# Performance work log

Hardware: AMD Instinct MI355X
Metric: run time of the kernel (lower is better)

Reference implementation:

```python
import jax, jax.numpy as jnp
import numpy as np

B, T, D = 128, 512, 400
N_VALS, N_ACTS = 1024, 128

def setup_inputs() -> dict:
    key = jax.random.key(0)
    ks = jax.random.split(key, 7)
    H_utt = jax.random.normal(ks[0], (B, T, D), dtype=jnp.float32)
    c_utt = jax.random.normal(ks[1], (B, D), dtype=jnp.float32)
    C_acts = jax.random.normal(ks[2], (B, N_ACTS, D), dtype=jnp.float32)
    C_vals = jax.random.normal(ks[3], (N_VALS, 1, D), dtype=jnp.float32)
    W_score = jax.random.normal(ks[4], (1, D), dtype=jnp.float32) * (1.0 / np.sqrt(D))
    b_score = jnp.zeros((1,), dtype=jnp.float32)
    lens = jax.random.randint(ks[5], (B,), T // 2, T + 1, dtype=jnp.int64 if jax.config.read('jax_enable_x64') else jnp.int32)
    lens = lens.at[0].set(T)  # ensure max(lens) == T so masking matches torch semantics
    return {"H_utt": H_utt, "c_utt": c_utt, "C_acts": C_acts, "C_vals": C_vals,
            "W_score": W_score, "b_score": b_score, "utterance_len": lens}

def reference(H_utt, c_utt, C_acts, C_vals, W_score, b_score, utterance_len):
    vals = C_vals[:, 0, :]                                   # [V, D]
    # --- y_utts: default attention of each value vector over utterance states ---
    scores = jnp.einsum('btd,vd->bvt', H_utt, vals)          # mul+sum scoring
    mask = jnp.arange(T)[None, :] < utterance_len[:, None]   # [B, T]
    scores = jnp.where(mask[:, None, :], scores, -jnp.inf)
    probs = jax.nn.softmax(scores, axis=-1)                  # [B, V, T]
    q_utts = jnp.einsum('bvt,btd->bvd', probs, H_utt)        # weighted sum contexts
    y_utts = jnp.einsum('bvd,d->bv', q_utts, W_score[0]) + b_score[0]  # utt_scorer
    # --- y_acts: attention of c_utt over per-example act vectors, then score vs vals ---
    s2 = jnp.einsum('bad,bd->ba', C_acts, c_utt)
    p2 = jax.nn.softmax(s2, axis=-1)
    q_acts = jnp.einsum('ba,bad->bd', p2, C_acts)            # [B, D]
    y_acts = q_acts @ vals.T                                 # [B, V]
    return (y_utts, y_acts)
```

## Files before the change

kernel.cpp:

```cpp
#include <hip/hip_runtime.h>
#include <hip/hip_bf16.h>

#define B_  128
#define T_  512
#define D_  400
#define NV  1024
#define NA  128

#define LDH  424
#define NT   32
#define MV   128
#define LOG2E 1.4426950408889634f

typedef __bf16 bf16_t;
typedef bf16_t bf16x8 __attribute__((ext_vector_type(8)));
typedef bf16_t bf16x4 __attribute__((ext_vector_type(4)));
typedef float  floatx4 __attribute__((ext_vector_type(4)));

__device__ inline void async_copy16(const void* g, void* l) {
    __builtin_amdgcn_global_load_lds(
        (const __attribute__((address_space(1))) unsigned int*)g,
        (__attribute__((address_space(3))) unsigned int*)l, 16, 0, 0);
}

__device__ inline float dot4(float4 a, float4 b) {
    return a.x * b.x + a.y * b.y + a.z * b.z + a.w * b.w;
}

template<int PRE>
__global__ __launch_bounds__(256) void prep_kernel(const float* __restrict__ H,
                                                   const float* __restrict__ W,
                                                   const float* __restrict__ cu,
                                                   const float* __restrict__ Ca,
                                                   float* __restrict__ hw,
                                                   bf16_t* __restrict__ Hbf,
                                                   float* __restrict__ q_ws) {
    __shared__ __align__(16) float4 cu4[100];
    __shared__ float s_lds[NA];
    __shared__ float p_lds[NA];
    __shared__ float red[8];
    __shared__ __align__(16) float4 part[100];

    int tid = threadIdx.x, wave = tid >> 6, lane = tid & 63;

    if (blockIdx.x >= 128) {
        long wid = (long)(blockIdx.x - 128) * 4 + wave;
        long r0 = wid * 8;
        const float* base = H + r0 * D_;
        float acc[8];
#pragma unroll
        for (int j = 0; j < 8; ++j) acc[j] = 0.f;

        if (lane < 50) {
            float4 wx = ((const float4*)W)[lane * 2];
            float4 wy = ((const float4*)W)[lane * 2 + 1];
            bf16_t* ob = Hbf + r0 * (long)LDH + lane * 8;
#pragma unroll
            for (int j = 0; j < 8; ++j) {
                const float4* p = (const float4*)(base + (long)j * D_ + lane * 8);
                float4 x = p[0], y = p[1];
                acc[j] = dot4(x, wx) + dot4(y, wy);
                if (PRE) {
                    bf16x8 f;
                    f[0] = (bf16_t)x.x; f[1] = (bf16_t)x.y;
                    f[2] = (bf16_t)x.z; f[3] = (bf16_t)x.w;
                    f[4] = (bf16_t)y.x; f[5] = (bf16_t)y.y;
                    f[6] = (bf16_t)y.z; f[7] = (bf16_t)y.w;
                    *(bf16x8*)(ob + (long)j * LDH) = f;
                }
            }
        } else if (PRE && lane < 53) {
            bf16x8 z;
#pragma unroll
            for (int jj = 0; jj < 8; ++jj) z[jj] = (bf16_t)0.0f;
            bf16_t* ob = Hbf + r0 * (long)LDH + lane * 8;
#pragma unroll
            for (int j = 0; j < 8; ++j)
                *(bf16x8*)(ob + (long)j * LDH) = z;
        }

#pragma unroll
        for (int off = 1; off < 64; off <<= 1) {
#pragma unroll
            for (int j = 0; j < 8; ++j) acc[j] += __shfl_xor(acc[j], off, 64);
        }
        if (lane == 0) {
#pragma unroll
            for (int j = 0; j < 8; ++j) hw[r0 + j] = acc[j];
        }
        return;
    }

    int b = blockIdx.x;

    if (tid < 100) cu4[tid] = ((const float4*)(cu + (size_t)b * D_))[tid];
    __syncthreads();

    const float4* Cb4 = (const float4*)(Ca + (size_t)b * NA * D_);
#pragma unroll 2
    for (int i = 0; i < 32; ++i) {
        int a = wave * 32 + i;
        const float4* row = Cb4 + (size_t)a * 100;
        float acc = dot4(row[lane], cu4[lane]);
        if (lane < 36) acc += dot4(row[lane + 64], cu4[lane + 64]);
#pragma unroll
        for (int off = 1; off < 64; off <<= 1) acc += __shfl_xor(acc, off, 64);
        if (lane == 0) s_lds[a] = acc;
    }
    __syncthreads();

    float s = (tid < NA) ? s_lds[tid] : -3.0e38f;
    float m = s;
#pragma unroll
    for (int off = 1; off < 64; off <<= 1) m = fmaxf(m, __shfl_xor(m, off, 64));
    if (lane == 0) red[wave] = m;
    __syncthreads();
    m = fmaxf(red[0], red[1]);
    float e = (tid < NA) ? __expf(s - m) : 0.f;
    float sum = e;
#pragma unroll
    for (int off = 1; off < 64; off <<= 1) sum += __shfl_xor(sum, off, 64);
    if (lane == 0) red[4 + wave] = sum;
    __syncthreads();
    float S = red[4] + red[5];
    if (tid < NA) p_lds[tid] = e / S;
    __syncthreads();

    int c4 = tid % 100;
    int half = tid / 100;
    float4 acc0 = {0.f, 0.f, 0.f, 0.f};
    if (tid < 200) {
        float4 acc1 = {0.f, 0.f, 0.f, 0.f};
        int a0 = half * 64;
#pragma unroll 4
        for (int a = 0; a < 64; a += 2) {
            float p0 = p_lds[a0 + a], p1 = p_lds[a0 + a + 1];
            float4 x0 = Cb4[(size_t)(a0 + a) * 100 + c4];
            float4 x1 = Cb4[(size_t)(a0 + a + 1) * 100 + c4];
            acc0.x += p0 * x0.x; acc0.y += p0 * x0.y; acc0.z += p0 * x0.z; acc0.w += p0 * x0.w;
            acc1.x += p1 * x1.x; acc1.y += p1 * x1.y; acc1.z += p1 * x1.z; acc1.w += p1 * x1.w;
        }
        acc0.x += acc1.x; acc0.y += acc1.y; acc0.z += acc1.z; acc0.w += acc1.w;
        if (half == 1) part[c4] = acc0;
    }
    __syncthreads();
    if (tid < 100) {
        float4 o = part[c4];
        o.x += acc0.x; o.y += acc0.y; o.z += acc0.z; o.w += acc0.w;
        ((float4*)(q_ws + (size_t)b * D_))[c4] = o;
    }
}

template<int PRE>
__global__ __launch_bounds__(256, 2) void main_kernel(const float* __restrict__ H,
                                                      const bf16_t* __restrict__ Hbf,
                                                      const float* __restrict__ Cv,
                                                      const float* __restrict__ hw,
                                                      const float* __restrict__ q_ws,
                                                      const float* __restrict__ bs,
                                                      const int* __restrict__ lens,
                                                      float* __restrict__ out) {
    __shared__ bf16_t h_lds[2][NT * LDH];

    int i = blockIdx.x;
    int xcd = i & 7, vc = (i >> 3) & 7, bb = i >> 6;
    int b = xcd + 8 * bb;
    int vbase = vc * MV;

    int tid = threadIdx.x;
    int wave = tid >> 6, lane = tid & 63;
    int lrow = lane & 15, quad = lane >> 4;

    int len = lens[b];
    float b0 = bs[0];

    if (!PRE) {
        for (int idx = tid; idx < 2 * NT * (LDH - D_); idx += 256) {
            int bu = idx / (NT * (LDH - D_));
            int rem = idx % (NT * (LDH - D_));
            int r = rem / (LDH - D_), c = rem % (LDH - D_);
            h_lds[bu][r * LDH + D_ + c] = (bf16_t)0.0f;
        }
    }

    bf16x8 afrag[2][13];
#pragma unroll
    for (int set = 0; set < 2; ++set) {
        const float* vrow = Cv + (size_t)(vbase + wave * 32 + set * 16 + lrow) * D_;
#pragma unroll
        for (int kk = 0; kk < 13; ++kk) {
            int k0 = kk * 32 + quad * 8;
            bf16x8 f;
            if (k0 >= D_) {
#pragma unroll
                for (int j = 0; j < 8; ++j) f[j] = (bf16_t)0.0f;
            } else {
                const float4* p = (const float4*)(vrow + k0);
                float4 x = p[0], y = p[1];
                f[0] = (bf16_t)(x.x * LOG2E); f[1] = (bf16_t)(x.y * LOG2E);
                f[2] = (bf16_t)(x.z * LOG2E); f[3] = (bf16_t)(x.w * LOG2E);
                f[4] = (bf16_t)(y.x * LOG2E); f[5] = (bf16_t)(y.y * LOG2E);
                f[6] = (bf16_t)(y.z * LOG2E); f[7] = (bf16_t)(y.w * LOG2E);
            }
            afrag[set][kk] = f;
        }
    }

    float m_s[2][4], l_s[2][4], a_s[2][4];
#pragma unroll
    for (int set = 0; set < 2; ++set)
#pragma unroll
        for (int r = 0; r < 4; ++r) { m_s[set][r] = -3.0e38f; l_s[set][r] = 0.f; a_s[set][r] = 0.f; }

    int ntiles = (len + NT - 1) / NT;
    const float* Hb = H + (size_t)b * T_ * D_;
    const bf16_t* Hbfb = Hbf + (size_t)b * T_ * LDH;
    const float* hwb = hw + (size_t)b * T_;

    auto stage = [&](int buf, int tt) {
        if (PRE) {
            const char* gt = (const char*)(Hbfb + (size_t)tt * NT * LDH);
            char* lt = (char*)h_lds[buf];
#pragma unroll 1
            for (int off = tid * 16; off < NT * LDH * 2; off += 4096)
                async_copy16(gt + off, lt + off);
        } else {
            for (int idx = tid; idx < NT * (D_ / 4); idx += 256) {
                int r = idx / (D_ / 4), c4 = idx % (D_ / 4);
                float4 x = *(const float4*)(Hb + (size_t)(tt * NT + r) * D_ + c4 * 4);
                bf16x4 f;
                f[0] = (bf16_t)x.x; f[1] = (bf16_t)x.y;
                f[2] = (bf16_t)x.z; f[3] = (bf16_t)x.w;
                *(bf16x4*)(&h_lds[buf][r * LDH + c4 * 4]) = f;
            }
        }
    };

    stage(0, 0);
    __syncthreads();

    for (int tt = 0; tt < ntiles; ++tt) {
        int cur = tt & 1;
        if (tt + 1 < ntiles) stage(cur ^ 1, tt + 1);

        int t0 = tt * NT;
        float hwv[2];
#pragma unroll
        for (int s = 0; s < 2; ++s) hwv[s] = hwb[t0 + s * 16 + lrow];

        floatx4 c[2][2];
        floatx4 zero4 = {0.f, 0.f, 0.f, 0.f};
#pragma unroll
        for (int set = 0; set < 2; ++set)
#pragma unroll
            for (int s = 0; s < 2; ++s) c[set][s] = zero4;

#pragma unroll
        for (int kk = 0; kk < 13; ++kk) {
            int koff = kk * 32 + quad * 8;
#pragma unroll
            for (int s = 0; s < 2; ++s) {
                bf16x8 bfr = *(const bf16x8*)(&h_lds[cur][(s * 16 + lrow) * LDH + koff]);
                c[0][s] = __builtin_amdgcn_mfma_f32_16x16x32_bf16(afrag[0][kk], bfr, c[0][s], 0, 0, 0);
                c[1][s] = __builtin_amdgcn_mfma_f32_16x16x32_bf16(afrag[1][kk], bfr, c[1][s], 0, 0, 0);
            }
        }

        if (t0 + NT > len) {
#pragma unroll
            for (int s = 0; s < 2; ++s) {
                int t = t0 + s * 16 + lrow;
                if (t >= len) {
#pragma unroll
                    for (int set = 0; set < 2; ++set) {
                        c[set][s][0] = -3.0e38f; c[set][s][1] = -3.0e38f;
                        c[set][s][2] = -3.0e38f; c[set][s][3] = -3.0e38f;
                    }
                }
            }
        }

#pragma unroll
        for (int set = 0; set < 2; ++set)
#pragma unroll
            for (int r = 0; r < 4; ++r) {
                float cm = fmaxf(c[set][0][r], c[set][1][r]);
                float mn = fmaxf(m_s[set][r], cm);
                float alpha = __builtin_amdgcn_exp2f(m_s[set][r] - mn);
                float ps = 0.f, qs = 0.f;
#pragma unroll
                for (int s = 0; s < 2; ++s) {
                    float p = __builtin_amdgcn_exp2f(c[set][s][r] - mn);
                    ps += p;
                    qs += p * hwv[s];
                }
                l_s[set][r] = l_s[set][r] * alpha + ps;
                a_s[set][r] = a_s[set][r] * alpha + qs;
                m_s[set][r] = mn;
            }

        __syncthreads();
    }

#pragma unroll
    for (int set = 0; set < 2; ++set)
#pragma unroll
        for (int r = 0; r < 4; ++r) {
            float m = m_s[set][r], l = l_s[set][r], a = a_s[set][r];
#pragma unroll
            for (int off = 1; off < 16; off <<= 1) {
                float mo = __shfl_xor(m, off, 64);
                float lo = __shfl_xor(l, off, 64);
                float ao = __shfl_xor(a, off, 64);
                float mn = fmaxf(m, mo);
                float f1 = __builtin_amdgcn_exp2f(m - mn);
                float f2 = __builtin_amdgcn_exp2f(mo - mn);
                l = l * f1 + lo * f2;
                a = a * f1 + ao * f2;
                m = mn;
            }
            if (lrow == 0) {
                int v = vbase + wave * 32 + set * 16 + quad * 4 + r;
                out[(size_t)b * NV + v] = a / l + b0;
            }
        }

    {
        const float4* q4 = (const float4*)(q_ws + (size_t)b * D_);
        float4 qa = q4[lane];
        float4 qb = (lane < 36) ? q4[lane + 64] : make_float4(0.f, 0.f, 0.f, 0.f);
#pragma unroll 1
        for (int ii = 0; ii < 32; ii += 4) {
            int v0 = vbase + wave * 32 + ii;
            float acc[4];
#pragma unroll
            for (int r = 0; r < 4; ++r) {
                const float4* v4 = (const float4*)(Cv + (size_t)(v0 + r) * D_);
                acc[r] = dot4(v4[lane], qa);
                if (lane < 36) acc[r] += dot4(v4[lane + 64], qb);
            }
#pragma unroll
            for (int off = 1; off < 64; off <<= 1) {
#pragma unroll
                for (int r = 0; r < 4; ++r) acc[r] += __shfl_xor(acc[r], off, 64);
            }
            if (lane == 0) {
                float4 o = make_float4(acc[0], acc[1], acc[2], acc[3]);
                *(float4*)(out + (size_t)B_ * NV + (size_t)b * NV + v0) = o;
            }
        }
    }
}

extern "C" void kernel_launch(void* const* d_in, const int* in_sizes, int n_in,
                              void* d_out, int out_size, void* d_ws, size_t ws_size,
                              hipStream_t stream) {
    const float* H    = (const float*)d_in[0];
    const float* cu   = (const float*)d_in[1];
    const float* Ca   = (const float*)d_in[2];
    const float* Cv   = (const float*)d_in[3];
    const float* W    = (const float*)d_in[4];
    const float* bs   = (const float*)d_in[5];
    const int*   lens = (const int*)d_in[6];
    float* out = (float*)d_out;

    float*  hw   = (float*)d_ws;
    float*  q_ws = hw + (size_t)B_ * T_;
    bf16_t* Hbf  = (bf16_t*)(q_ws + (size_t)B_ * D_);

    size_t need = ((size_t)B_ * T_ + (size_t)B_ * D_) * sizeof(float)
                + (size_t)B_ * T_ * LDH * sizeof(bf16_t);
    bool pre = (ws_size >= need);

    dim3 pgrid(128 + 2048);
    if (pre) {
        prep_kernel<1><<<pgrid, dim3(256), 0, stream>>>(H, W, cu, Ca, hw, Hbf, q_ws);
        main_kernel<1><<<dim3(1024), dim3(256), 0, stream>>>(H, Hbf, Cv, hw, q_ws, bs, lens, out);
    } else {
        prep_kernel<0><<<pgrid, dim3(256), 0, stream>>>(H, W, cu, Ca, hw, Hbf, q_ws);
        main_kernel<0><<<dim3(1024), dim3(256), 0, stream>>>(H, Hbf, Cv, hw, q_ws, bs, lens, out);
    }
}
```

Baseline: 309.7 us.

## Drop bf16 pre-conversion of H and convert fp32 tiles in-kernel

Removes the path where the prep kernel writes a padded bf16 copy of H to workspace and the main kernel async-copies it into LDS. The main kernel now always loads fp32 H tiles directly, converting to bf16 with 8-element vector stores into LDS. This avoids writing and re-reading a ~55MB intermediate, but each of the 8 value-chunk blocks per batch now reads fp32 H (twice the bytes of bf16) and loses the asynchronous global-to-LDS copy, so staging may stall compute.

```diff
diff --git a/kernel.cpp b/kernel.cpp
--- a/kernel.cpp
+++ b/kernel.cpp
@@ -14,26 +14,17 @@
 
 typedef __bf16 bf16_t;
 typedef bf16_t bf16x8 __attribute__((ext_vector_type(8)));
-typedef bf16_t bf16x4 __attribute__((ext_vector_type(4)));
 typedef float  floatx4 __attribute__((ext_vector_type(4)));
-
-__device__ inline void async_copy16(const void* g, void* l) {
-    __builtin_amdgcn_global_load_lds(
-        (const __attribute__((address_space(1))) unsigned int*)g,
-        (__attribute__((address_space(3))) unsigned int*)l, 16, 0, 0);
-}
 
 __device__ inline float dot4(float4 a, float4 b) {
     return a.x * b.x + a.y * b.y + a.z * b.z + a.w * b.w;
 }
 
-template<int PRE>
 __global__ __launch_bounds__(256) void prep_kernel(const float* __restrict__ H,
                                                    const float* __restrict__ W,
                                                    const float* __restrict__ cu,
                                                    const float* __restrict__ Ca,
                                                    float* __restrict__ hw,
-                                                   bf16_t* __restrict__ Hbf,
                                                    float* __restrict__ q_ws) {
     __shared__ __align__(16) float4 cu4[100];
     __shared__ float s_lds[NA];
@@ -54,31 +45,12 @@
         if (lane < 50) {
             float4 wx = ((const float4*)W)[lane * 2];
             float4 wy = ((const float4*)W)[lane * 2 + 1];
-            bf16_t* ob = Hbf + r0 * (long)LDH + lane * 8;
 #pragma unroll
             for (int j = 0; j < 8; ++j) {
                 const float4* p = (const float4*)(base + (long)j * D_ + lane * 8);
-                float4 x = p[0], y = p[1];
-                acc[j] = dot4(x, wx) + dot4(y, wy);
-                if (PRE) {
-                    bf16x8 f;
-                    f[0] = (bf16_t)x.x; f[1] = (bf16_t)x.y;
-                    f[2] = (bf16_t)x.z; f[3] = (bf16_t)x.w;
-                    f[4] = (bf16_t)y.x; f[5] = (bf16_t)y.y;
-                    f[6] = (bf16_t)y.z; f[7] = (bf16_t)y.w;
-                    *(bf16x8*)(ob + (long)j * LDH) = f;
-                }
-            }
-        } else if (PRE && lane < 53) {
-            bf16x8 z;
-#pragma unroll
-            for (int jj = 0; jj < 8; ++jj) z[jj] = (bf16_t)0.0f;
-            bf16_t* ob = Hbf + r0 * (long)LDH + lane * 8;
-#pragma unroll
-            for (int j = 0; j < 8; ++j)
-                *(bf16x8*)(ob + (long)j * LDH) = z;
-        }
-
+                acc[j] = dot4(p[0], wx) + dot4(p[1], wy);
+            }
+        }
 #pragma unroll
         for (int off = 1; off < 64; off <<= 1) {
 #pragma unroll
@@ -151,9 +123,7 @@
     }
 }
 
-template<int PRE>
 __global__ __launch_bounds__(256, 2) void main_kernel(const float* __restrict__ H,
-                                                      const bf16_t* __restrict__ Hbf,
                                                       const float* __restrict__ Cv,
                                                       const float* __restrict__ hw,
                                                       const float* __restrict__ q_ws,
@@ -174,13 +144,11 @@
     int len = lens[b];
     float b0 = bs[0];
 
-    if (!PRE) {
-        for (int idx = tid; idx < 2 * NT * (LDH - D_); idx += 256) {
-            int bu = idx / (NT * (LDH - D_));
-            int rem = idx % (NT * (LDH - D_));
-            int r = rem / (LDH - D_), c = rem % (LDH - D_);
-            h_lds[bu][r * LDH + D_ + c] = (bf16_t)0.0f;
-        }
+    for (int idx = tid; idx < 2 * NT * (LDH - D_); idx += 256) {
+        int bu = idx / (NT * (LDH - D_));
+        int rem = idx % (NT * (LDH - D_));
+        int r = rem / (LDH - D_), c = rem % (LDH - D_);
+        h_lds[bu][r * LDH + D_ + c] = (bf16_t)0.0f;
     }
 
     bf16x8 afrag[2][13];
@@ -214,34 +182,26 @@
 
     int ntiles = (len + NT - 1) / NT;
     const float* Hb = H + (size_t)b * T_ * D_;
-    const bf16_t* Hbfb = Hbf + (size_t)b * T_ * LDH;
     const float* hwb = hw + (size_t)b * T_;
 
-    auto stage = [&](int buf, int tt) {
-        if (PRE) {
-            const char* gt = (const char*)(Hbfb + (size_t)tt * NT * LDH);
-            char* lt = (char*)h_lds[buf];
-#pragma unroll 1
-            for (int off = tid * 16; off < NT * LDH * 2; off += 4096)
-                async_copy16(gt + off, lt + off);
-        } else {
-            for (int idx = tid; idx < NT * (D_ / 4); idx += 256) {
-                int r = idx / (D_ / 4), c4 = idx % (D_ / 4);
-                float4 x = *(const float4*)(Hb + (size_t)(tt * NT + r) * D_ + c4 * 4);
-                bf16x4 f;
-                f[0] = (bf16_t)x.x; f[1] = (bf16_t)x.y;
-                f[2] = (bf16_t)x.z; f[3] = (bf16_t)x.w;
-                *(bf16x4*)(&h_lds[buf][r * LDH + c4 * 4]) = f;
-            }
+    auto stage_f32 = [&](int buf, int tt) {
+        for (int idx = tid; idx < NT * 50; idx += 256) {
+            int r = idx / 50, c = idx - r * 50;
+            const float4* s = (const float4*)(Hb + (size_t)(tt * NT + r) * D_ + c * 8);
+            float4 x = s[0], y = s[1];
+            bf16x8 f;
+            f[0] = (bf16_t)x.x; f[1] = (bf16_t)x.y; f[2] = (bf16_t)x.z; f[3] = (bf16_t)x.w;
+            f[4] = (bf16_t)y.x; f[5] = (bf16_t)y.y; f[6] = (bf16_t)y.z; f[7] = (bf16_t)y.w;
+            *(bf16x8*)((char*)h_lds[buf] + r * 848 + c * 16) = f;
         }
     };
 
-    stage(0, 0);
+    stage_f32(0, 0);
     __syncthreads();
 
     for (int tt = 0; tt < ntiles; ++tt) {
         int cur = tt & 1;
-        if (tt + 1 < ntiles) stage(cur ^ 1, tt + 1);
+        if (tt + 1 < ntiles) stage_f32(cur ^ 1, tt + 1);
 
         int t0 = tt * NT;
         float hwv[2];
@@ -364,20 +324,9 @@
     const int*   lens = (const int*)d_in[6];
     float* out = (float*)d_out;
 
-    float*  hw   = (float*)d_ws;
-    float*  q_ws = hw + (size_t)B_ * T_;
-    bf16_t* Hbf  = (bf16_t*)(q_ws + (size_t)B_ * D_);
-
-    size_t need = ((size_t)B_ * T_ + (size_t)B_ * D_) * sizeof(float)
-                + (size_t)B_ * T_ * LDH * sizeof(bf16_t);
-    bool pre = (ws_size >= need);
-
-    dim3 pgrid(128 + 2048);
-    if (pre) {
-        prep_kernel<1><<<pgrid, dim3(256), 0, stream>>>(H, W, cu, Ca, hw, Hbf, q_ws);
-        main_kernel<1><<<dim3(1024), dim3(256), 0, stream>>>(H, Hbf, Cv, hw, q_ws, bs, lens, out);
-    } else {
-        prep_kernel<0><<<pgrid, dim3(256), 0, stream>>>(H, W, cu, Ca, hw, Hbf, q_ws);
-        main_kernel<0><<<dim3(1024), dim3(256), 0, stream>>>(H, Hbf, Cv, hw, q_ws, bs, lens, out);
-    }
+    float* hw   = (float*)d_ws;
+    float* q_ws = hw + (size_t)B_ * T_;
+
+    prep_kernel<<<dim3(128 + 2048), dim3(256), 0, stream>>>(H, W, cu, Ca, hw, q_ws);
+    main_kernel<<<dim3(1024), dim3(256), 0, stream>>>(H, Cv, hw, q_ws, bs, lens, out);
 }
```

After: 349.3 us. +12.8%, slower.

## Swizzle bf16 H layout in LDS and halve value tile per block

Applied to the files above, without the earlier changes.

Shrinks the padded bf16 H row stride to 416 and applies an XOR swizzle on 16-byte chunks, both when writing Hbf in the prep kernel and when staging and reading tiles from LDS. The aim is to avoid LDS bank conflicts on the MFMA B-fragment reads. It also halves the value rows per block (MV 128 to 64), doubling the grid to 2048 blocks, and cuts per-wave accumulators so occupancy can rise to 3 blocks per CU. The cost is that each H tile is now streamed twice as many times across blocks, raising L2/HBM traffic.

```diff
diff --git a/kernel.cpp b/kernel.cpp
--- a/kernel.cpp
+++ b/kernel.cpp
@@ -7,14 +7,13 @@
 #define NV  1024
 #define NA  128
 
-#define LDH  424
+#define LDH  416
 #define NT   32
-#define MV   128
+#define MV   64
 #define LOG2E 1.4426950408889634f
 
 typedef __bf16 bf16_t;
 typedef bf16_t bf16x8 __attribute__((ext_vector_type(8)));
-typedef bf16_t bf16x4 __attribute__((ext_vector_type(4)));
 typedef float  floatx4 __attribute__((ext_vector_type(4)));
 
 __device__ inline void async_copy16(const void* g, void* l) {
@@ -54,7 +53,8 @@
         if (lane < 50) {
             float4 wx = ((const float4*)W)[lane * 2];
             float4 wy = ((const float4*)W)[lane * 2 + 1];
-            bf16_t* ob = Hbf + r0 * (long)LDH + lane * 8;
+            bf16_t* ob = Hbf + r0 * (long)LDH;
+            int pos = lane;
 #pragma unroll
             for (int j = 0; j < 8; ++j) {
                 const float4* p = (const float4*)(base + (long)j * D_ + lane * 8);
@@ -66,10 +66,11 @@
                     f[2] = (bf16_t)x.z; f[3] = (bf16_t)x.w;
                     f[4] = (bf16_t)y.x; f[5] = (bf16_t)y.y;
                     f[6] = (bf16_t)y.z; f[7] = (bf16_t)y.w;
-                    *(bf16x8*)(ob + (long)j * LDH) = f;
+                    int pj = (lane < 48) ? (pos ^ j) : pos;
+                    *(bf16x8*)(ob + (long)j * LDH + pj * 8) = f;
                 }
             }
-        } else if (PRE && lane < 53) {
+        } else if (PRE && lane < 52) {
             bf16x8 z;
 #pragma unroll
             for (int jj = 0; jj < 8; ++jj) z[jj] = (bf16_t)0.0f;
@@ -152,7 +153,7 @@
 }
 
 template<int PRE>
-__global__ __launch_bounds__(256, 2) void main_kernel(const float* __restrict__ H,
+__global__ __launch_bounds__(256, 3) void main_kernel(const float* __restrict__ H,
                                                       const bf16_t* __restrict__ Hbf,
                                                       const float* __restrict__ Cv,
                                                       const float* __restrict__ hw,
@@ -163,7 +164,7 @@
     __shared__ bf16_t h_lds[2][NT * LDH];
 
     int i = blockIdx.x;
-    int xcd = i & 7, vc = (i >> 3) & 7, bb = i >> 6;
+    int xcd = i & 7, vc = (i >> 3) & 15, bb = i >> 7;
     int b = xcd + 8 * bb;
     int vbase = vc * MV;
 
@@ -175,18 +176,19 @@
     float b0 = bs[0];
 
     if (!PRE) {
-        for (int idx = tid; idx < 2 * NT * (LDH - D_); idx += 256) {
-            int bu = idx / (NT * (LDH - D_));
-            int rem = idx % (NT * (LDH - D_));
-            int r = rem / (LDH - D_), c = rem % (LDH - D_);
-            h_lds[bu][r * LDH + D_ + c] = (bf16_t)0.0f;
-        }
-    }
-
-    bf16x8 afrag[2][13];
-#pragma unroll
-    for (int set = 0; set < 2; ++set) {
-        const float* vrow = Cv + (size_t)(vbase + wave * 32 + set * 16 + lrow) * D_;
+        for (int idx = tid; idx < 2 * NT * 2; idx += 256) {
+            int bu = idx >> 6, rem = idx & 63;
+            int r = rem >> 1, c = 50 + (rem & 1);
+            bf16x8 z;
+#pragma unroll
+            for (int j = 0; j < 8; ++j) z[j] = (bf16_t)0.0f;
+            *(bf16x8*)((char*)h_lds[bu] + r * 832 + c * 16) = z;
+        }
+    }
+
+    bf16x8 afrag[13];
+    {
+        const float* vrow = Cv + (size_t)(vbase + wave * 16 + lrow) * D_;
 #pragma unroll
         for (int kk = 0; kk < 13; ++kk) {
             int k0 = kk * 32 + quad * 8;
@@ -202,15 +204,13 @@
                 f[4] = (bf16_t)(y.x * LOG2E); f[5] = (bf16_t)(y.y * LOG2E);
                 f[6] = (bf16_t)(y.z * LOG2E); f[7] = (bf16_t)(y.w * LOG2E);
             }
-            afrag[set][kk] = f;
-        }
-    }
-
-    float m_s[2][4], l_s[2][4], a_s[2][4];
-#pragma unroll
-    for (int set = 0; set < 2; ++set)
-#pragma unroll
-        for (int r = 0; r < 4; ++r) { m_s[set][r] = -3.0e38f; l_s[set][r] = 0.f; a_s[set][r] = 0.f; }
+            afrag[kk] = f;
+        }
+    }
+
+    float m_s[4], l_s[4], a_s[4];
+#pragma unroll
+    for (int r = 0; r < 4; ++r) { m_s[r] = -3.0e38f; l_s[r] = 0.f; a_s[r] = 0.f; }
 
     int ntiles = (len + NT - 1) / NT;
     const float* Hb = H + (size_t)b * T_ * D_;
@@ -225,19 +225,25 @@
             for (int off = tid * 16; off < NT * LDH * 2; off += 4096)
                 async_copy16(gt + off, lt + off);
         } else {
-            for (int idx = tid; idx < NT * (D_ / 4); idx += 256) {
-                int r = idx / (D_ / 4), c4 = idx % (D_ / 4);
-                float4 x = *(const float4*)(Hb + (size_t)(tt * NT + r) * D_ + c4 * 4);
-                bf16x4 f;
-                f[0] = (bf16_t)x.x; f[1] = (bf16_t)x.y;
-                f[2] = (bf16_t)x.z; f[3] = (bf16_t)x.w;
-                *(bf16x4*)(&h_lds[buf][r * LDH + c4 * 4]) = f;
+            for (int idx = tid; idx < NT * 50; idx += 256) {
+                int r = idx / 50, c = idx - r * 50;
+                const float4* s = (const float4*)(Hb + (size_t)(tt * NT + r) * D_ + c * 8);
+                float4 x = s[0], y = s[1];
+                bf16x8 f;
+                f[0] = (bf16_t)x.x; f[1] = (bf16_t)x.y; f[2] = (bf16_t)x.z; f[3] = (bf16_t)x.w;
+                f[4] = (bf16_t)y.x; f[5] = (bf16_t)y.y; f[6] = (bf16_t)y.z; f[7] = (bf16_t)y.w;
+                int pos = (c < 48) ? (c ^ (r & 7)) : c;
+                *(bf16x8*)((char*)h_lds[buf] + r * 832 + pos * 16) = f;
             }
         }
     };
 
     stage(0, 0);
     __syncthreads();
+
+    const int swz = (lrow & 7) << 4;
+    const int rowb0 = lrow * 832;
+    const int rowb1 = (16 + lrow) * 832;
 
     for (int tt = 0; tt < ntiles; ++tt) {
         int cur = tt & 1;
@@ -248,90 +254,72 @@
 #pragma unroll
         for (int s = 0; s < 2; ++s) hwv[s] = hwb[t0 + s * 16 + lrow];
 
-        floatx4 c[2][2];
-        floatx4 zero4 = {0.f, 0.f, 0.f, 0.f};
-#pragma unroll
-        for (int set = 0; set < 2; ++set)
-#pragma unroll
-            for (int s = 0; s < 2; ++s) c[set][s] = zero4;
-
+        floatx4 c0 = {0.f, 0.f, 0.f, 0.f};
+        floatx4 c1 = {0.f, 0.f, 0.f, 0.f};
+
+        const char* L = (const char*)h_lds[cur];
 #pragma unroll
         for (int kk = 0; kk < 13; ++kk) {
-            int koff = kk * 32 + quad * 8;
-#pragma unroll
-            for (int s = 0; s < 2; ++s) {
-                bf16x8 bfr = *(const bf16x8*)(&h_lds[cur][(s * 16 + lrow) * LDH + koff]);
-                c[0][s] = __builtin_amdgcn_mfma_f32_16x16x32_bf16(afrag[0][kk], bfr, c[0][s], 0, 0, 0);
-                c[1][s] = __builtin_amdgcn_mfma_f32_16x16x32_bf16(afrag[1][kk], bfr, c[1][s], 0, 0, 0);
-            }
+            int koffb = kk * 64 + quad * 16;
+            int o = (kk < 12) ? (koffb ^ swz) : koffb;
+            bf16x8 f0 = *(const bf16x8*)(L + rowb0 + o);
+            c0 = __builtin_amdgcn_mfma_f32_16x16x32_bf16(afrag[kk], f0, c0, 0, 0, 0);
+            bf16x8 f1 = *(const bf16x8*)(L + rowb1 + o);
+            c1 = __builtin_amdgcn_mfma_f32_16x16x32_bf16(afrag[kk], f1, c1, 0, 0, 0);
         }
 
         if (t0 + NT > len) {
-#pragma unroll
-            for (int s = 0; s < 2; ++s) {
-                int t = t0 + s * 16 + lrow;
-                if (t >= len) {
-#pragma unroll
-                    for (int set = 0; set < 2; ++set) {
-                        c[set][s][0] = -3.0e38f; c[set][s][1] = -3.0e38f;
-                        c[set][s][2] = -3.0e38f; c[set][s][3] = -3.0e38f;
-                    }
-                }
-            }
-        }
-
-#pragma unroll
-        for (int set = 0; set < 2; ++set)
-#pragma unroll
-            for (int r = 0; r < 4; ++r) {
-                float cm = fmaxf(c[set][0][r], c[set][1][r]);
-                float mn = fmaxf(m_s[set][r], cm);
-                float alpha = __builtin_amdgcn_exp2f(m_s[set][r] - mn);
-                float ps = 0.f, qs = 0.f;
-#pragma unroll
-                for (int s = 0; s < 2; ++s) {
-                    float p = __builtin_amdgcn_exp2f(c[set][s][r] - mn);
-                    ps += p;
-                    qs += p * hwv[s];
-                }
-                l_s[set][r] = l_s[set][r] * alpha + ps;
-                a_s[set][r] = a_s[set][r] * alpha + qs;
-                m_s[set][r] = mn;
-            }
+            if (t0 + lrow >= len) {
+                c0[0] = -3.0e38f; c0[1] = -3.0e38f; c0[2] = -3.0e38f; c0[3] = -3.0e38f;
+            }
+            if (t0 + 16 + lrow >= len) {
+                c1[0] = -3.0e38f; c1[1] = -3.0e38f; c1[2] = -3.0e38f; c1[3] = -3.0e38f;
+            }
+        }
+
+#pragma unroll
+        for (int r = 0; r < 4; ++r) {
+            float cm = fmaxf(c0[r], c1[r]);
+            float mn = fmaxf(m_s[r], cm);
+            float alpha = __builtin_amdgcn_exp2f(m_s[r] - mn);
+            float p0 = __builtin_amdgcn_exp2f(c0[r] - mn);
+            float p1 = __builtin_amdgcn_exp2f(c1[r] - mn);
+            l_s[r] = l_s[r] * alpha + p0 + p1;
+            a_s[r] = a_s[r] * alpha + p0 * hwv[0] + p1 * hwv[1];
+            m_s[r] = mn;
+        }
 
         __syncthreads();
     }
 
 #pragma unroll
-    for (int set = 0; set < 2; ++set)
-#pragma unroll
-        for (int r = 0; r < 4; ++r) {
-            float m = m_s[set][r], l = l_s[set][r], a = a_s[set][r];
-#pragma unroll
-            for (int off = 1; off < 16; off <<= 1) {
-                float mo = __shfl_xor(m, off, 64);
-                float lo = __shfl_xor(l, off, 64);
-                float ao = __shfl_xor(a, off, 64);
-                float mn = fmaxf(m, mo);
-                float f1 = __builtin_amdgcn_exp2f(m - mn);
-                float f2 = __builtin_amdgcn_exp2f(mo - mn);
-                l = l * f1 + lo * f2;
-                a = a * f1 + ao * f2;
-                m = mn;
-            }
-            if (lrow == 0) {
-                int v = vbase + wave * 32 + set * 16 + quad * 4 + r;
-                out[(size_t)b * NV + v] = a / l + b0;
-            }
-        }
+    for (int r = 0; r < 4; ++r) {
+        float m = m_s[r], l = l_s[r], a = a_s[r];
+#pragma unroll
+        for (int off = 1; off < 16; off <<= 1) {
+            float mo = __shfl_xor(m, off, 64);
+            float lo = __shfl_xor(l, off, 64);
+            float ao = __shfl_xor(a, off, 64);
+            float mn = fmaxf(m, mo);
+            float f1 = __builtin_amdgcn_exp2f(m - mn);
+            float f2 = __builtin_amdgcn_exp2f(mo - mn);
+            l = l * f1 + lo * f2;
+            a = a * f1 + ao * f2;
+            m = mn;
+        }
+        if (lrow == 0) {
+            int v = vbase + wave * 16 + quad * 4 + r;
+            out[(size_t)b * NV + v] = a / l + b0;
+        }
+    }
 
     {
         const float4* q4 = (const float4*)(q_ws + (size_t)b * D_);
         float4 qa = q4[lane];
         float4 qb = (lane < 36) ? q4[lane + 64] : make_float4(0.f, 0.f, 0.f, 0.f);
 #pragma unroll 1
-        for (int ii = 0; ii < 32; ii += 4) {
-            int v0 = vbase + wave * 32 + ii;
+        for (int ii = 0; ii < 16; ii += 4) {
+            int v0 = vbase + wave * 16 + ii;
             float acc[4];
 #pragma unroll
             for (int r = 0; r < 4; ++r) {
@@ -375,9 +363,9 @@
     dim3 pgrid(128 + 2048);
     if (pre) {
         prep_kernel<1><<<pgrid, dim3(256), 0, stream>>>(H, W, cu, Ca, hw, Hbf, q_ws);
-        main_kernel<1><<<dim3(1024), dim3(256), 0, stream>>>(H, Hbf, Cv, hw, q_ws, bs, lens, out);
+        main_kernel<1><<<dim3(2048), dim3(256), 0, stream>>>(H, Hbf, Cv, hw, q_ws, bs, lens, out);
     } else {
         prep_kernel<0><<<pgrid, dim3(256), 0, stream>>>(H, W, cu, Ca, hw, Hbf, q_ws);
-        main_kernel<0><<<dim3(1024), dim3(256), 0, stream>>>(H, Hbf, Cv, hw, q_ws, bs, lens, out);
-    }
-}
+        main_kernel<0><<<dim3(2048), dim3(256), 0, stream>>>(H, Hbf, Cv, hw, q_ws, bs, lens, out);
+    }
+}
```

Result: no change. 308.5 us (-0.4%).
